# Kernel tuning notes

Measured on AMD Instinct MI355X. Metric: run time of the kernel, lower is better.

## Reference

```python
import jax, jax.numpy as jnp
import numpy as np

B, N = 16, 80
TEXT_DIM, AUDIO_DIM = 1024, 512
FD, FO = 512, 512          # bilinear pooling D, O
DH = 384                   # hidden_dim
L = 2                      # gnn_layers
NC = 7                     # num_class
IN_DIM = DH * (L + 1) + FO # out_mlp input dim


def _w(key, shape, scale=0.02):
    return (jax.random.normal(key, shape, dtype=jnp.float32) * scale)


def setup_inputs() -> dict:
    key = jax.random.key(0)
    ks = list(jax.random.split(key, 40))
    inp = {
        "features_text": jax.random.normal(ks[0], (B, N, TEXT_DIM), dtype=jnp.float32),
        "features_audio": jax.random.normal(ks[1], (B, N, AUDIO_DIM), dtype=jnp.float32),
        "adj": jnp.ones((B, N, N), dtype=jnp.int32),
        "s_mask": jax.random.randint(ks[2], (B, N, N), 0, 2, dtype=jnp.int32),
        "s_mask_onehot": jnp.zeros((B, N, N, 2), dtype=jnp.float32),
        "lengths": jnp.full((N and B,), N, dtype=jnp.int64) if False else jnp.full((B,), N, dtype=jnp.int32),
        # bilinear pooling
        "U1_w": _w(ks[3], (FD, TEXT_DIM)),
        "U2_w": _w(ks[4], (FD, AUDIO_DIM)),
        "P_w": _w(ks[5], (FO, FD)), "P_b": jnp.zeros((FO,), jnp.float32),
        "V1_w": _w(ks[6], (FO, TEXT_DIM)),
        "V2_w": _w(ks[7], (FO, AUDIO_DIM)),
        # fc1
        "fc1_w": _w(ks[8], (DH, FO)), "fc1_b": jnp.zeros((DH,), jnp.float32),
        # per-layer GAT (stacked on leading layer dim)
        "gat_w": _w(ks[9], (L, 1, 2 * DH)), "gat_b": jnp.zeros((L, 1), jnp.float32),
        "Wr0": _w(ks[10], (L, DH, DH)), "Wr1": _w(ks[11], (L, DH, DH)),
        # GRU cells (torch GRUCell layout: weight_ih (3H,H), weight_hh (3H,H))
        "gruC_wi": _w(ks[12], (L, 3 * DH, DH)), "gruC_wh": _w(ks[13], (L, 3 * DH, DH)),
        "gruC_bi": jnp.zeros((L, 3 * DH), jnp.float32), "gruC_bh": jnp.zeros((L, 3 * DH), jnp.float32),
        "gruP_wi": _w(ks[14], (L, 3 * DH, DH)), "gruP_wh": _w(ks[15], (L, 3 * DH, DH)),
        "gruP_bi": jnp.zeros((L, 3 * DH), jnp.float32), "gruP_bh": jnp.zeros((L, 3 * DH), jnp.float32),
        # out_mlp: Linear(in_dim,H) ReLU, Linear(H,H) ReLU, Linear(H,NC)
        "mlp_w0": _w(ks[16], (DH, IN_DIM)), "mlp_b0": jnp.zeros((DH,), jnp.float32),
        "mlp_w1": _w(ks[17], (DH, DH)), "mlp_b1": jnp.zeros((DH,), jnp.float32),
        "mlp_w2": _w(ks[18], (NC, DH)), "mlp_b2": jnp.zeros((NC,), jnp.float32),
    }
    return inp


def _gru_cell(x, h, wi, wh, bi, bh):
    gi = x @ wi.T + bi
    gh = h @ wh.T + bh
    i_r, i_z, i_n = jnp.split(gi, 3, axis=-1)
    h_r, h_z, h_n = jnp.split(gh, 3, axis=-1)
    r = jax.nn.sigmoid(i_r + h_r)
    z = jax.nn.sigmoid(i_z + h_z)
    n = jnp.tanh(i_n + r * h_n)
    return (1.0 - z) * n + z * h


def reference(features_text, features_audio, adj, s_mask, s_mask_onehot, lengths,
              U1_w, U2_w, P_w, P_b, V1_w, V2_w, fc1_w, fc1_b,
              gat_w, gat_b, Wr0, Wr1,
              gruC_wi, gruC_wh, gruC_bi, gruC_bh,
              gruP_wi, gruP_wh, gruP_bi, gruP_bh,
              mlp_w0, mlp_b0, mlp_w1, mlp_b1, mlp_w2, mlp_b2):
    # bilinear pooling fusion
    c_ = jax.nn.sigmoid(features_text @ U1_w.T) * jax.nn.sigmoid(features_audio @ U2_w.T)
    fused = c_ @ P_w.T + P_b + features_text @ V1_w.T + features_audio @ V2_w.T  # (B,N,FO)
    H0 = jax.nn.relu(fused @ fc1_w.T + fc1_b)                                    # (B,N,DH)

    n = H0.shape[1]
    adj_f = adj.astype(H0.dtype)
    s_f = s_mask.astype(H0.dtype)
    pos = jnp.arange(n)
    adj_t = jnp.swapaxes(adj_f, 0, 1)  # (N,B,N)
    s_t = jnp.swapaxes(s_f, 0, 1)      # (N,B,N)

    Hs = [H0]
    for l in range(gat_w.shape[0]):
        wq, wk = gat_w[l, 0, :H0.shape[2]], gat_w[l, 0, H0.shape[2]:]
        gb = gat_b[l, 0]
        wr0, wr1 = Wr0[l], Wr1[l]
        cwi, cwh, cbi, cbh = gruC_wi[l], gruC_wh[l], gruC_bi[l], gruC_bh[l]
        pwi, pwh, pbi, pbh = gruP_wi[l], gruP_wh[l], gruP_bi[l], gruP_bh[l]
        Hl = Hs[-1]

        def step(H1, xs):
            xi, adj_i, s_i, i = xs                              # xi (B,DH)
            # GAT_dialoggcn_v1 score: linear(cat(Q,K))
            alpha = (xi @ wq)[:, None] + H1 @ wk + gb           # (B,N)
            mask = adj_i * (pos < i).astype(alpha.dtype)        # only past, adj-allowed
            alpha = alpha - (1.0 - mask) * 1e30
            w = jax.nn.softmax(alpha, axis=-1)                  # (B,N)
            sm = s_i[..., None]
            V = (H1 @ wr0.T) * sm + (H1 @ wr1.T) * (1.0 - sm)   # (B,N,DH)
            M = jnp.einsum('bn,bnd->bd', w, V)
            M = jnp.where(i == 0, jnp.zeros_like(M), M)         # i=0: no attention, M=0
            C = _gru_cell(xi, M, cwi, cwh, cbi, cbh)
            P = _gru_cell(M, xi, pwi, pwh, pbi, pbh)
            Hnew = C + P
            H1 = jax.lax.dynamic_update_slice(H1, Hnew[:, None, :], (0, i, 0))
            return H1, Hnew

        xs = (jnp.swapaxes(Hl, 0, 1), adj_t, s_t, jnp.arange(n))
        _, ys = jax.lax.scan(step, jnp.zeros_like(Hl), xs)
        Hs.append(jnp.swapaxes(ys, 0, 1))

    Hcat = jnp.concatenate(Hs + [fused], axis=2)  # (B,N,IN_DIM)
    # attentive_node_features with nodal_att_type=None is identity; dropout eval = identity
    h = jax.nn.relu(Hcat @ mlp_w0.T + mlp_b0)
    h = jax.nn.relu(h @ mlp_w1.T + mlp_b1)
    logits = h @ mlp_w2.T + mlp_b2
    return jax.nn.log_softmax(logits, axis=2)
```

## Files before the change

kernel.cpp:

```cpp
#include <hip/hip_runtime.h>
#include <hip/hip_bf16.h>
#include <math.h>

#define BB 16
#define NN 80
#define DH_ 384
#define LDH 1664

typedef unsigned int uint;
typedef unsigned long long u64;
typedef __attribute__((ext_vector_type(8))) short short8;
typedef __attribute__((ext_vector_type(4))) float f32x4;

__device__ __forceinline__ uint packbf(float lo, float hi)
{
    uint a = __float_as_uint(lo);
    a = (a + 0x7fffu + ((a >> 16) & 1u)) >> 16;
    uint b = __float_as_uint(hi);
    b = (b + 0x7fffu + ((b >> 16) & 1u)) & 0xffff0000u;
    return a | b;
}
__device__ __forceinline__ float bflo(uint u) { return __uint_as_float(u << 16); }
__device__ __forceinline__ float bfhi(uint u) { return __uint_as_float(u & 0xffff0000u); }
__device__ __forceinline__ unsigned short cvt1(float f)
{
    uint a = __float_as_uint(f);
    return (unsigned short)((a + 0x7fffu + ((a >> 16) & 1u)) >> 16);
}

__global__ __launch_bounds__(256)
void gemm_mfma(const float* __restrict__ A, int lda,
               const unsigned short* __restrict__ W, int ldw,
               const float* __restrict__ bias,
               float* __restrict__ C, int ldc,
               int K, int act, int accum)
{
    __shared__ __attribute__((aligned(16))) unsigned short As[4096];
    __shared__ __attribute__((aligned(16))) unsigned short Bs[4096];
    const int t = threadIdx.x;
    const int lane = t & 63, wave = t >> 6;
    const int r0 = blockIdx.y * 64, o0 = blockIdx.x * 64;

    f32x4 acc0 = {0.f, 0.f, 0.f, 0.f};
    f32x4 acc1 = acc0, acc2 = acc0, acc3 = acc0;

    const int srow = t >> 2;
    const int scp = (t & 3) * 2;
    const int sw0 = ((scp ^ (srow & 7))) * 8;
    const int sw1 = (((scp + 1) ^ (srow & 7))) * 8;
    const float* ap0 = A + (size_t)(r0 + srow) * lda + scp * 8;
    const unsigned short* bp0 = W + (size_t)(o0 + srow) * ldw + scp * 8;

    const int fr = lane & 15, kg = lane >> 4;
    const int fsw = fr & 7;
    const int arow = (wave * 16 + fr) * 64;

    for (int kb = 0; kb < K; kb += 64) {
        float4 a0 = *(const float4*)(ap0 + kb);
        float4 a1 = *(const float4*)(ap0 + kb + 4);
        float4 a2 = *(const float4*)(ap0 + kb + 8);
        float4 a3 = *(const float4*)(ap0 + kb + 12);
        uint4 b0 = *(const uint4*)(bp0 + kb);
        uint4 b1 = *(const uint4*)(bp0 + kb + 8);
        uint4 apk0, apk1;
        apk0.x = packbf(a0.x, a0.y); apk0.y = packbf(a0.z, a0.w);
        apk0.z = packbf(a1.x, a1.y); apk0.w = packbf(a1.z, a1.w);
        apk1.x = packbf(a2.x, a2.y); apk1.y = packbf(a2.z, a2.w);
        apk1.z = packbf(a3.x, a3.y); apk1.w = packbf(a3.z, a3.w);
        *(uint4*)&As[srow * 64 + sw0] = apk0;
        *(uint4*)&As[srow * 64 + sw1] = apk1;
        *(uint4*)&Bs[srow * 64 + sw0] = b0;
        *(uint4*)&Bs[srow * 64 + sw1] = b1;
        __syncthreads();
#pragma unroll
        for (int h = 0; h < 2; ++h) {
            int ach = kg + 4 * h;
            short8 af = *(const short8*)&As[arow + ((ach ^ fsw)) * 8];
            short8 bf0 = *(const short8*)&Bs[(0 * 16 + fr) * 64 + ((ach ^ fsw)) * 8];
            short8 bf1 = *(const short8*)&Bs[(1 * 16 + fr) * 64 + ((ach ^ fsw)) * 8];
            short8 bf2 = *(const short8*)&Bs[(2 * 16 + fr) * 64 + ((ach ^ fsw)) * 8];
            short8 bf3 = *(const short8*)&Bs[(3 * 16 + fr) * 64 + ((ach ^ fsw)) * 8];
            acc0 = __builtin_amdgcn_mfma_f32_16x16x32_bf16(af, bf0, acc0, 0, 0, 0);
            acc1 = __builtin_amdgcn_mfma_f32_16x16x32_bf16(af, bf1, acc1, 0, 0, 0);
            acc2 = __builtin_amdgcn_mfma_f32_16x16x32_bf16(af, bf2, acc2, 0, 0, 0);
            acc3 = __builtin_amdgcn_mfma_f32_16x16x32_bf16(af, bf3, acc3, 0, 0, 0);
        }
        __syncthreads();
    }
    const int rg = lane >> 4;
    f32x4 av[4] = {acc0, acc1, acc2, acc3};
#pragma unroll
    for (int c = 0; c < 4; ++c) {
        int col = o0 + c * 16 + fr;
        float bv = bias ? bias[col] : 0.f;
#pragma unroll
        for (int r = 0; r < 4; ++r) {
            int row = r0 + wave * 16 + rg * 4 + r;
            float v = av[c][r] + bv;
            if (accum) v += C[(size_t)row * ldc + col];
            if (act == 1) v = fmaxf(v, 0.f);
            else if (act == 2) v = 1.f / (1.f + expf(-v));
            else if (act == 3 && col < 512) v = 1.f / (1.f + expf(-v));
            C[(size_t)row * ldc + col] = v;
        }
    }
}

__global__ void wcvt(const float* __restrict__ U1, const float* __restrict__ V1,
                     const float* __restrict__ U2, const float* __restrict__ V2,
                     const float* __restrict__ Pw, const float* __restrict__ fc1w,
                     const float* __restrict__ cwi, const float* __restrict__ pwh,
                     const float* __restrict__ w0, const float* __restrict__ w1,
                     const float* __restrict__ cbi, const float* __restrict__ pbh,
                     unsigned short* __restrict__ wB, float* __restrict__ gb_)
{
    int idx = blockIdx.x * 256 + threadIdx.x;
    if (idx < 4587520) {
        float v;
        if      (idx < 524288)  v = U1[idx];
        else if (idx < 1048576) v = V1[idx - 524288];
        else if (idx < 1310720) v = U2[idx - 1048576];
        else if (idx < 1572864) v = V2[idx - 1310720];
        else if (idx < 1835008) v = Pw[idx - 1572864];
        else if (idx < 2031616) v = fc1w[idx - 1835008];
        else if (idx < 2473984) v = cwi[idx - 2031616];
        else if (idx < 2916352) v = pwh[idx - 2473984];
        else if (idx < 3358720) v = cwi[442368 + idx - 2916352];
        else if (idx < 3801088) v = pwh[442368 + idx - 3358720];
        else if (idx < 4440064) v = w0[idx - 3801088];
        else                    v = w1[idx - 4440064];
        wB[idx] = cvt1(v);
    } else if (idx < 4592128) {
        int j = idx - 4587520;
        int l = j / 2304, o = j % 2304;
        gb_[j] = (o < 1152) ? cbi[l * 1152 + o] : pbh[l * 1152 + o - 1152];
    }
}

__global__ void ew2(const float* __restrict__ T1, const float* __restrict__ T2,
                    float* __restrict__ CBuf, float* __restrict__ Hc)
{
    int idx = blockIdx.x * 256 + threadIdx.x;
    int r = idx >> 9, c = idx & 511;
    CBuf[idx] = T1[r * 1024 + c] * T2[r * 1024 + c];
    Hc[r * LDH + 1152 + c] = T1[r * 1024 + 512 + c] + T2[r * 1024 + 512 + c];
}

__global__ void trans_wg3(const float* __restrict__ cwh, const float* __restrict__ pwi,
                          uint* __restrict__ WgPk)
{
    int idx = blockIdx.x * 256 + threadIdx.x;
    int l = idx / 442368;
    int r = idx % 442368;
    int g = r / 27648;
    int r2 = r % 27648;
    int k = r2 / 72, cp = r2 % 72;
    float v[2];
#pragma unroll
    for (int u = 0; u < 2; ++u) {
        int c = 2 * cp + u;
        int idx6 = c / 24, o = c % 24, d = g * 24 + o;
        v[u] = (idx6 < 3) ? cwh[l * 442368 + (idx6 * 384 + d) * 384 + k]
                          : pwi[l * 442368 + ((idx6 - 3) * 384 + d) * 384 + k];
    }
    WgPk[idx] = packbf(v[0], v[1]);
}

__global__ void trans_wr3(const float* __restrict__ Wr0, const float* __restrict__ Wr1,
                          uint* __restrict__ WrPk)
{
    int idx = blockIdx.x * 256 + threadIdx.x;
    int l = idx / 147456;
    int r = idx % 147456;
    int g = r / 9216;
    int r2 = r % 9216;
    int k = r2 / 24, dl = r2 % 24;
    int row = g * 24 + dl;
    float w0 = Wr0[l * 147456 + row * 384 + k];
    float w1 = Wr1[l * 147456 + row * 384 + k];
    WrPk[idx] = packbf(w0, w1);
}

__global__ __launch_bounds__(256)
void qpre_k(const float* __restrict__ Hc, int hin, const float* __restrict__ wq,
            float* __restrict__ q)
{
    int wave = threadIdx.x >> 6, lane = threadIdx.x & 63;
    int row = blockIdx.x * 4 + wave;
    const float* hp = Hc + row * LDH + hin;
    float s = 0.f;
#pragma unroll
    for (int u = 0; u < 6; ++u) s = fmaf(hp[lane + 64 * u], wq[lane + 64 * u], s);
#pragma unroll
    for (int m = 1; m < 64; m <<= 1) s += __shfl_xor(s, m);
    if (lane == 0) q[row] = s;
}

#define ALD64(p)    __hip_atomic_load((p), __ATOMIC_RELAXED, __HIP_MEMORY_SCOPE_AGENT)
#define AST64(p, v) __hip_atomic_store((p), (v), __ATOMIC_RELAXED, __HIP_MEMORY_SCOPE_AGENT)

__global__ __launch_bounds__(512)
void scan10(float* Hc, int hin, int hout,
            const float* __restrict__ gPre,
            const uint* __restrict__ WrPkl,
            const uint* __restrict__ WgPkl,
            const float* __restrict__ qpre,
            const float* __restrict__ gatwl,
            const float* __restrict__ gatbl,
            const int* __restrict__ adj,
            const int* __restrict__ smask,
            const float* __restrict__ cbh,
            const float* __restrict__ pbi,
            u64* __restrict__ X1,
            u64* __restrict__ X2)
{
    const int wg = blockIdx.x;
    const int b = wg >> 4, g = wg & 15;
    const int t = threadIdx.x;

    extern __shared__ uint WgL[];
    __shared__ uint WrL[384 * 25];
    __shared__ uint Pc16[NN][25];
    __shared__ float kvS[NN];
    __shared__ float2 ws01[NN];
    __shared__ float Mv[DH_];
    __shared__ float uA[864];
    __shared__ float gs[144];
    __shared__ float karr[16];

    {
        const uint* src = WgPkl + g * 27648;
        for (int idx = t; idx < 27648; idx += 512) WgL[idx] = src[idx];
        const uint* src2 = WrPkl + g * 9216;
        for (int idx = t; idx < 9216; idx += 512) {
            int k = idx / 24, dl = idx % 24;
            WrL[k * 25 + dl] = src2[idx];
        }
    }
    __syncthreads();

    u64* X1b = X1 + b * 1024;
    u64* X2b = X2 + b * 512;
    const float gb = gatbl[0];

    int ca0 = 0, cs0 = 0, ca1 = 0, cs1 = 0;
    float cq = 0.f;
    int na0 = 0, ns0 = 0, na1 = 0, ns1 = 0;
    float nq = 0.f;
    float gpv = 0.f, xv = 0.f;

    for (int i = 0; i < NN; ++i) {
        const int rowi = b * NN + i;

        if (t < 144) gpv = gPre[rowi * 2304 + (t / 24) * 384 + g * 24 + (t % 24)];
        else if (t < 168) xv = Hc[rowi * LDH + hin + g * 24 + (t - 144)];
        if (t < 64) {
            int ip = (i + 1 < NN) ? (i + 1) : (NN - 1);
            int rp = b * NN + ip;
            na0 = adj[rp * NN + t];
            ns0 = smask[rp * NN + t];
            if (t + 64 < NN) { na1 = adj[rp * NN + t + 64]; ns1 = smask[rp * NN + t + 64]; }
            nq = qpre[rp];
        }
        __syncthreads();

        if (i > 0) {
            const u64* Xs2 = X2b + ((i - 1) & 1) * 256;
            if (t < 256) {
                int gg = t >> 4, j = t & 15;
                if (j < 13) {
                    u64 w;
                    do { w = ALD64(&Xs2[gg * 16 + j]); } while ((uint)(w >> 32) != (uint)i);
                    uint lo = (uint)w;
                    if (j < 12) {
                        uA[gg * 24 + 2 * j]     = bflo(lo);
                        uA[gg * 24 + 2 * j + 1] = bfhi(lo);
                    } else {
                        karr[gg] = __uint_as_float(lo);
                    }
                }
            }
            __syncthreads();

            if (t == 400) {
                float s = 0.f;
#pragma unroll
                for (int u = 0; u < 16; ++u) s += karr[u];
                kvS[i - 1] = s;
            }
            if (t < 384) {
                int dl0 = t >> 4, sub = t & 15, part = sub & 7, half = sub >> 3;
                float acc = 0.f;
#pragma unroll 8
                for (int m = 0; m < 48; ++m) {
                    int k = part + 8 * m;
                    uint u = WrL[k * 25 + dl0];
                    float w2_ = half ? bfhi(u) : bflo(u);
                    acc = fmaf(w2_, uA[k], acc);
                }
                acc += __shfl_xor(acc, 1);
                acc += __shfl_xor(acc, 2);
                acc += __shfl_xor(acc, 4);
                float other = __shfl_xor(acc, 8);
                if (sub == 0) Pc16[i - 1][dl0] = packbf(acc, other);
            }
            __syncthreads();

            if (t < 64) {
                float q = cq + gb;
                int j0 = t, j1 = t + 64;
                float a0v = -1e30f, a1v = -1e30f;
                if (j0 < i && ca0 != 0) a0v = q + kvS[j0];
                if (j1 < i && ca1 != 0) a1v = q + kvS[j1];
                float mx = fmaxf(a0v, a1v);
#pragma unroll
                for (int m = 1; m < 64; m <<= 1) mx = fmaxf(mx, __shfl_xor(mx, m));
                float e0 = expf(a0v - mx);
                float e1 = (j1 < NN) ? expf(a1v - mx) : 0.f;
                float ss = e0 + e1;
#pragma unroll
                for (int m = 1; m < 64; m <<= 1) ss += __shfl_xor(ss, m);
                float inv = 1.f / ss;
                float w0 = e0 * inv;
                float s0 = (float)cs0;
                ws01[j0] = make_float2(w0 * s0, w0 - w0 * s0);
                if (j1 < NN) {
                    float w1 = e1 * inv;
                    float s1 = (float)cs1;
                    ws01[j1] = make_float2(w1 * s1, w1 - w1 * s1);
                }
            }
            __syncthreads();

            u64* Xs1 = X1b + (i & 1) * 512;
            if (t < 384) {
                int dl0 = t >> 4, sub = t & 15;
                float acc = 0.f;
                for (int j = sub; j < i; j += 16) {
                    uint u = Pc16[j][dl0];
                    float2 w2_ = ws01[j];
                    acc = fmaf(w2_.x, bflo(u), acc);
                    acc = fmaf(w2_.y, bfhi(u), acc);
                }
                acc += __shfl_xor(acc, 1);
                acc += __shfl_xor(acc, 2);
                acc += __shfl_xor(acc, 4);
                acc += __shfl_xor(acc, 8);
                if (sub == 0)
                    AST64(&Xs1[g * 32 + dl0],
                          ((u64)(uint)(i + 1) << 32) | (u64)__float_as_uint(acc));
            }

            if (t < 512) {
                int gg = t >> 5, j = t & 31;
                if (j < 24) {
                    u64 wm;
                    do { wm = ALD64(&Xs1[gg * 32 + j]); } while ((uint)(wm >> 32) != (uint)(i + 1));
                    Mv[gg * 24 + j] = __uint_as_float((uint)wm);
                }
            }
            __syncthreads();
        } else {
            if (t < 384) Mv[t] = 0.f;
            __syncthreads();
        }

        if (t < 64) { ca0 = na0; cs0 = ns0; ca1 = na1; cs1 = ns1; cq = nq; }

        if (t < 432) {
            int cp = t % 72, kt = t / 72;
            int kbase = kt * 64;
            float a0 = 0.f, a1 = 0.f;
#pragma unroll 8
            for (int kk = 0; kk < 64; ++kk) {
                uint u = WgL[(kbase + kk) * 72 + cp];
                float m = Mv[kbase + kk];
                a0 = fmaf(bflo(u), m, a0);
                a1 = fmaf(bfhi(u), m, a1);
            }
            uA[kt * 144 + 2 * cp] = a0;
            uA[kt * 144 + 2 * cp + 1] = a1;
        }
        __syncthreads();
        if (t < 144) {
            float s = 0.f;
#pragma unroll
            for (int kt = 0; kt < 6; ++kt) s += uA[kt * 144 + t];
            gs[t] = s;
        }
        __syncthreads();

        if (t < 144) uA[t] = gpv;
        else if (t < 168) uA[t] = xv;
        __syncthreads();

        u64* Xs2w = X2b + (i & 1) * 256;
        if (t < 32) {
            float kp = 0.f, h = 0.f;
            if (t < 24) {
                int dg = g * 24 + t;
                float m = Mv[dg];
                float gir = uA[t], giz = uA[24 + t], gin = uA[48 + t];
                float ghr = gs[t] + cbh[dg];
                float ghz = gs[24 + t] + cbh[384 + dg];
                float ghn = gs[48 + t] + cbh[768 + dg];
                float r = 1.f / (1.f + expf(-(gir + ghr)));
                float z = 1.f / (1.f + expf(-(giz + ghz)));
                float n = tanhf(gin + r * ghn);
                float Cc = (1.f - z) * n + z * m;
                float pir = gs[72 + t] + pbi[dg];
                float piz = gs[96 + t] + pbi[384 + dg];
                float pin = gs[120 + t] + pbi[768 + dg];
                float phr = uA[72 + t], phz = uA[96 + t], phn = uA[120 + t];
                float r2 = 1.f / (1.f + expf(-(pir + phr)));
                float z2 = 1.f / (1.f + expf(-(piz + phz)));
                float n2 = tanhf(pin + r2 * phn);
                float x = uA[144 + t];
                float Pp = (1.f - z2) * n2 + z2 * x;
                h = Cc + Pp;
                Hc[rowi * LDH + hout + dg] = h;
                kp = h * gatwl[384 + dg];
            }
            int src = (t < 12) ? 2 * t : 0;
            float ha = __shfl(h, src);
            float hb = __shfl(h, src + 1);
            if (t < 12)
                AST64(&Xs2w[g * 16 + t],
                      ((u64)(uint)(i + 1) << 32) | (u64)packbf(ha, hb));
#pragma unroll
            for (int m = 16; m >= 1; m >>= 1) kp += __shfl_down(kp, m);
            if (t == 0)
                AST64(&Xs2w[g * 16 + 12],
                      ((u64)(uint)(i + 1) << 32) | (u64)__float_as_uint(kp));
        }
    }
}

__global__ __launch_bounds__(256)
void mlp_final(const float* __restrict__ h, const float* __restrict__ w2,
               const float* __restrict__ b2, float* __restrict__ out)
{
    int wave = threadIdx.x >> 6, lane = threadIdx.x & 63;
    int r = blockIdx.x * 4 + wave;
    float hreg[6];
#pragma unroll
    for (int m = 0; m < 6; ++m) hreg[m] = h[r * 384 + lane + 64 * m];
    float logit[7];
#pragma unroll
    for (int c = 0; c < 7; ++c) {
        float s = 0.f;
#pragma unroll
        for (int m = 0; m < 6; ++m)
            s = fmaf(hreg[m], w2[c * 384 + lane + 64 * m], s);
#pragma unroll
        for (int m = 1; m < 64; m <<= 1) s += __shfl_xor(s, m);
        logit[c] = s + b2[c];
    }
    float mx = logit[0];
#pragma unroll
    for (int c = 1; c < 7; ++c) mx = fmaxf(mx, logit[c]);
    float se = 0.f;
#pragma unroll
    for (int c = 0; c < 7; ++c) se += expf(logit[c] - mx);
    float lse = mx + logf(se);
    if (lane < 7) out[r * 7 + lane] = logit[lane] - lse;
}

extern "C" void kernel_launch(void* const* d_in, const int* in_sizes, int n_in,
                              void* d_out, int out_size, void* d_ws, size_t ws_size,
                              hipStream_t stream)
{
    const float* ftext = (const float*)d_in[0];
    const float* faud  = (const float*)d_in[1];
    const int*   adj   = (const int*)d_in[2];
    const int*   smask = (const int*)d_in[3];
    const float* U1    = (const float*)d_in[6];
    const float* U2    = (const float*)d_in[7];
    const float* Pw    = (const float*)d_in[8];
    const float* Pb    = (const float*)d_in[9];
    const float* V1    = (const float*)d_in[10];
    const float* V2    = (const float*)d_in[11];
    const float* fc1w  = (const float*)d_in[12];
    const float* fc1b  = (const float*)d_in[13];
    const float* gatw  = (const float*)d_in[14];
    const float* gatb  = (const float*)d_in[15];
    const float* Wr0   = (const float*)d_in[16];
    const float* Wr1   = (const float*)d_in[17];
    const float* cwi   = (const float*)d_in[18];
    const float* cwh   = (const float*)d_in[19];
    const float* cbi   = (const float*)d_in[20];
    const float* cbh   = (const float*)d_in[21];
    const float* pwi   = (const float*)d_in[22];
    const float* pwh   = (const float*)d_in[23];
    const float* pbi   = (const float*)d_in[24];
    const float* pbh   = (const float*)d_in[25];
    const float* w0    = (const float*)d_in[26];
    const float* b0    = (const float*)d_in[27];
    const float* w1    = (const float*)d_in[28];
    const float* b1    = (const float*)d_in[29];
    const float* w2    = (const float*)d_in[30];
    const float* b2    = (const float*)d_in[31];
    float* out = (float*)d_out;
    float* ws = (float*)d_ws;

    float* Hcat  = ws;
    float* gPre  = ws + 2129920;
    float* T1b   = gPre;
    float* T2b   = gPre + 1310720;
    float* CBuf  = ws + 5079040;
    uint*  WgPk  = (uint*)(ws + 5734400);
    uint*  WrPk  = (uint*)(ws + 6619136);
    float* gb_   = ws + 6914048;
    float* qpreB = ws + 6918656;
    u64*   X1l0  = (u64*)(ws + 6921216);
    u64*   X2l0  = X1l0 + 16384;
    u64*   X1l1  = X2l0 + 8192;
    u64*   X2l1  = X1l1 + 16384;
    unsigned short* wB = (unsigned short*)(ws + 7019520);

    auto g = [&](const float* A, int lda, size_t woff, int ldw,
                 const float* bias, float* C, int ldc, int K, int N,
                 int act, int accum) {
        dim3 grid(N / 64, 1280 / 64);
        gemm_mfma<<<grid, 256, 0, stream>>>(A, lda, wB + woff, ldw, bias, C, ldc,
                                            K, act, accum);
    };

    hipMemsetAsync(X1l0, 0, (size_t)(16384 + 8192) * 2 * sizeof(u64), stream);

    wcvt<<<17938, 256, 0, stream>>>(U1, V1, U2, V2, Pw, fc1w, cwi, pwh, w0, w1,
                                    cbi, pbh, wB, gb_);
    trans_wg3<<<3456, 256, 0, stream>>>(cwh, pwi, WgPk);
    trans_wr3<<<1152, 256, 0, stream>>>(Wr0, Wr1, WrPk);

    g(ftext, 1024, 0, 1024, nullptr, T1b, 1024, 1024, 1024, 3, 0);
    g(faud, 512, 1048576, 512, nullptr, T2b, 1024, 512, 1024, 3, 0);
    ew2<<<2560, 256, 0, stream>>>(T1b, T2b, CBuf, Hcat);
    g(CBuf, 512, 1572864, 512, Pb, Hcat + 1152, LDH, 512, 512, 0, 1);
    g(Hcat + 1152, LDH, 1835008, 512, fc1b, Hcat, LDH, 512, 384, 1, 0);

    for (int l = 0; l < 2; ++l) {
        g(Hcat + l * 384, LDH, 2031616 + (size_t)l * 884736, 384,
          gb_ + l * 2304, gPre, 2304, 384, 2304, 0, 0);
        qpre_k<<<320, 256, 0, stream>>>(Hcat, l * 384, gatw + l * 768, qpreB + l * 1280);
        scan10<<<256, 512, 110592, stream>>>(Hcat, l * 384, (l + 1) * 384, gPre,
                                             WrPk + l * 147456, WgPk + l * 442368,
                                             qpreB + l * 1280, gatw + l * 768, gatb + l,
                                             adj, smask, cbh + l * 1152, pbi + l * 1152,
                                             l ? X1l1 : X1l0, l ? X2l1 : X2l0);
    }

    g(Hcat, LDH, 3801088, 1664, b0, CBuf, 384, 1664, 384, 1, 0);
    g(CBuf, 384, 4440064, 384, b1, gPre, 384, 384, 384, 1, 0);
    mlp_final<<<320, 256, 0, stream>>>(gPre, w2, b2, out);
}
```

Baseline: 1.153 ms.

## Overlap attention softmax with exchange wait and pack M exchange into bf16 pairs

The scan kernel now computes the GAT key sum and the softmax weights in wave 0 at the same time as the other waves poll the cross-workgroup exchange for the GRU partial vector. This removes one block-wide barrier and a serial single-thread reduction from each step. The attention output M exchanged between workgroups is packed two values per 64-bit slot as bf16, which halves the polling traffic and the size of the exchange buffer. The cost is reduced precision for M in the recurrent dependency chain.

```diff
diff --git a/kernel.cpp b/kernel.cpp
--- a/kernel.cpp
+++ b/kernel.cpp
@@ -200,7 +200,7 @@
 #define AST64(p, v) __hip_atomic_store((p), (v), __ATOMIC_RELAXED, __HIP_MEMORY_SCOPE_AGENT)
 
 __global__ __launch_bounds__(512)
-void scan10(float* Hc, int hin, int hout,
+void scan11(float* Hc, int hin, int hout,
             const float* __restrict__ gPre,
             const uint* __restrict__ WrPkl,
             const uint* __restrict__ WgPkl,
@@ -214,8 +214,7 @@
             u64* __restrict__ X1,
             u64* __restrict__ X2)
 {
-    const int wg = blockIdx.x;
-    const int b = wg >> 4, g = wg & 15;
+    const int b = blockIdx.x >> 4, g = blockIdx.x & 15;
     const int t = threadIdx.x;
 
     extern __shared__ uint WgL[];
@@ -226,7 +225,6 @@
     __shared__ float Mv[DH_];
     __shared__ float uA[864];
     __shared__ float gs[144];
-    __shared__ float karr[16];
 
     {
         const uint* src = WgPkl + g * 27648;
@@ -239,7 +237,7 @@
     }
     __syncthreads();
 
-    u64* X1b = X1 + b * 1024;
+    u64* X1b = X1 + b * 512;
     u64* X2b = X2 + b * 512;
     const float gb = gatbl[0];
 
@@ -266,28 +264,49 @@
 
         if (i > 0) {
             const u64* Xs2 = X2b + ((i - 1) & 1) * 256;
-            if (t < 256) {
-                int gg = t >> 4, j = t & 15;
-                if (j < 13) {
+            if (t < 64) {
+                float kvnew = 0.f;
+                if (t < 16) {
                     u64 w;
-                    do { w = ALD64(&Xs2[gg * 16 + j]); } while ((uint)(w >> 32) != (uint)i);
-                    uint lo = (uint)w;
-                    if (j < 12) {
-                        uA[gg * 24 + 2 * j]     = bflo(lo);
-                        uA[gg * 24 + 2 * j + 1] = bfhi(lo);
-                    } else {
-                        karr[gg] = __uint_as_float(lo);
-                    }
+                    do { w = ALD64(&Xs2[t * 16 + 12]); } while ((uint)(w >> 32) != (uint)i);
+                    kvnew = __uint_as_float((uint)w);
                 }
+#pragma unroll
+                for (int m = 1; m < 64; m <<= 1) kvnew += __shfl_xor(kvnew, m);
+                if (t == 0) kvS[i - 1] = kvnew;
+                float q = cq + gb;
+                int j0 = t, j1 = t + 64;
+                float a0v = -1e30f, a1v = -1e30f;
+                if (j0 < i && ca0 != 0) a0v = q + ((j0 == i - 1) ? kvnew : kvS[j0]);
+                if (j1 < i && ca1 != 0) a1v = q + ((j1 == i - 1) ? kvnew : kvS[j1]);
+                float mx = fmaxf(a0v, a1v);
+#pragma unroll
+                for (int m = 1; m < 64; m <<= 1) mx = fmaxf(mx, __shfl_xor(mx, m));
+                float e0 = expf(a0v - mx);
+                float e1 = (j1 < NN) ? expf(a1v - mx) : 0.f;
+                float ss = e0 + e1;
+#pragma unroll
+                for (int m = 1; m < 64; m <<= 1) ss += __shfl_xor(ss, m);
+                float inv = 1.f / ss;
+                float w0 = e0 * inv;
+                float s0 = (float)cs0;
+                ws01[j0] = make_float2(w0 * s0, w0 - w0 * s0);
+                if (j1 < NN) {
+                    float w1 = e1 * inv;
+                    float s1 = (float)cs1;
+                    ws01[j1] = make_float2(w1 * s1, w1 - w1 * s1);
+                }
+            } else if (t < 256) {
+                int idx = t - 64;
+                int gg = idx / 12, j = idx % 12;
+                u64 w;
+                do { w = ALD64(&Xs2[gg * 16 + j]); } while ((uint)(w >> 32) != (uint)i);
+                uint lo = (uint)w;
+                uA[gg * 24 + 2 * j]     = bflo(lo);
+                uA[gg * 24 + 2 * j + 1] = bfhi(lo);
             }
             __syncthreads();
 
-            if (t == 400) {
-                float s = 0.f;
-#pragma unroll
-                for (int u = 0; u < 16; ++u) s += karr[u];
-                kvS[i - 1] = s;
-            }
             if (t < 384) {
                 int dl0 = t >> 4, sub = t & 15, part = sub & 7, half = sub >> 3;
                 float acc = 0.f;
@@ -306,35 +325,9 @@
             }
             __syncthreads();
 
-            if (t < 64) {
-                float q = cq + gb;
-                int j0 = t, j1 = t + 64;
-                float a0v = -1e30f, a1v = -1e30f;
-                if (j0 < i && ca0 != 0) a0v = q + kvS[j0];
-                if (j1 < i && ca1 != 0) a1v = q + kvS[j1];
-                float mx = fmaxf(a0v, a1v);
-#pragma unroll
-                for (int m = 1; m < 64; m <<= 1) mx = fmaxf(mx, __shfl_xor(mx, m));
-                float e0 = expf(a0v - mx);
-                float e1 = (j1 < NN) ? expf(a1v - mx) : 0.f;
-                float ss = e0 + e1;
-#pragma unroll
-                for (int m = 1; m < 64; m <<= 1) ss += __shfl_xor(ss, m);
-                float inv = 1.f / ss;
-                float w0 = e0 * inv;
-                float s0 = (float)cs0;
-                ws01[j0] = make_float2(w0 * s0, w0 - w0 * s0);
-                if (j1 < NN) {
-                    float w1 = e1 * inv;
-                    float s1 = (float)cs1;
-                    ws01[j1] = make_float2(w1 * s1, w1 - w1 * s1);
-                }
-            }
-            __syncthreads();
-
-            u64* Xs1 = X1b + (i & 1) * 512;
+            u64* Xs1 = X1b + (i & 1) * 256;
             if (t < 384) {
-                int dl0 = t >> 4, sub = t & 15;
+                int dl0 = t >> 4, sub = t & 15, lane6 = t & 63;
                 float acc = 0.f;
                 for (int j = sub; j < i; j += 16) {
                     uint u = Pc16[j][dl0];
@@ -346,18 +339,19 @@
                 acc += __shfl_xor(acc, 2);
                 acc += __shfl_xor(acc, 4);
                 acc += __shfl_xor(acc, 8);
-                if (sub == 0)
-                    AST64(&Xs1[g * 32 + dl0],
-                          ((u64)(uint)(i + 1) << 32) | (u64)__float_as_uint(acc));
+                float hi = __shfl(acc, (lane6 + 16) & 63);
+                if (sub == 0 && !(dl0 & 1))
+                    AST64(&Xs1[g * 16 + (dl0 >> 1)],
+                          ((u64)(uint)(i + 1) << 32) | (u64)packbf(acc, hi));
             }
 
-            if (t < 512) {
-                int gg = t >> 5, j = t & 31;
-                if (j < 24) {
-                    u64 wm;
-                    do { wm = ALD64(&Xs1[gg * 32 + j]); } while ((uint)(wm >> 32) != (uint)(i + 1));
-                    Mv[gg * 24 + j] = __uint_as_float((uint)wm);
-                }
+            if (t < 192) {
+                int gg = t / 12, j = t % 12;
+                u64 wm;
+                do { wm = ALD64(&Xs1[gg * 16 + j]); } while ((uint)(wm >> 32) != (uint)(i + 1));
+                uint lo = (uint)wm;
+                Mv[gg * 24 + 2 * j]     = bflo(lo);
+                Mv[gg * 24 + 2 * j + 1] = bfhi(lo);
             }
             __syncthreads();
         } else {
@@ -513,9 +507,9 @@
     float* gb_   = ws + 6914048;
     float* qpreB = ws + 6918656;
     u64*   X1l0  = (u64*)(ws + 6921216);
-    u64*   X2l0  = X1l0 + 16384;
+    u64*   X2l0  = X1l0 + 8192;
     u64*   X1l1  = X2l0 + 8192;
-    u64*   X2l1  = X1l1 + 16384;
+    u64*   X2l1  = X1l1 + 8192;
     unsigned short* wB = (unsigned short*)(ws + 7019520);
 
     auto g = [&](const float* A, int lda, size_t woff, int ldw,
@@ -526,7 +520,7 @@
                                             K, act, accum);
     };
 
-    hipMemsetAsync(X1l0, 0, (size_t)(16384 + 8192) * 2 * sizeof(u64), stream);
+    hipMemsetAsync(X1l0, 0, (size_t)4 * 8192 * sizeof(u64), stream);
 
     wcvt<<<17938, 256, 0, stream>>>(U1, V1, U2, V2, Pw, fc1w, cwi, pwh, w0, w1,
                                     cbi, pbh, wB, gb_);
@@ -543,7 +537,7 @@
         g(Hcat + l * 384, LDH, 2031616 + (size_t)l * 884736, 384,
           gb_ + l * 2304, gPre, 2304, 384, 2304, 0, 0);
         qpre_k<<<320, 256, 0, stream>>>(Hcat, l * 384, gatw + l * 768, qpreB + l * 1280);
-        scan10<<<256, 512, 110592, stream>>>(Hcat, l * 384, (l + 1) * 384, gPre,
+        scan11<<<256, 512, 110592, stream>>>(Hcat, l * 384, (l + 1) * 384, gPre,
                                              WrPk + l * 147456, WgPk + l * 442368,
                                              qpreB + l * 1280, gatw + l * 768, gatb + l,
                                              adj, smask, cbh + l * 1152, pbi + l * 1152,
```

After: 1.242 ms. 7.7% more time.
